# Kernel tuning notes

Measured on AMD Instinct MI355X. Metric: run time of the kernel, lower is better.

## Reference

```python
import jax, jax.numpy as jnp
import numpy as np

D_MODEL = 1024
N_HEADS = 16
D_K = D_MODEL // N_HEADS


def setup_inputs() -> dict:
    key = jax.random.key(0)
    ks = jax.random.split(key, 12)
    B, S = 2, 2048
    scale = 1.0 / np.sqrt(D_MODEL)
    inp = {
        "query": jax.random.normal(ks[0], (B, S, D_MODEL), jnp.float32),
        "key": jax.random.normal(ks[1], (B, S, D_MODEL), jnp.float32),
        "value": jax.random.normal(ks[2], (B, S, D_MODEL), jnp.float32),
        "weights": jax.random.uniform(ks[3], (B, S), jnp.float32),
        "wq": jax.random.normal(ks[4], (D_MODEL, D_MODEL), jnp.float32) * scale,
        "bq": jnp.zeros((D_MODEL,), jnp.float32),
        "wk": jax.random.normal(ks[5], (D_MODEL, D_MODEL), jnp.float32) * scale,
        "bk": jnp.zeros((D_MODEL,), jnp.float32),
        "wv": jax.random.normal(ks[6], (D_MODEL, D_MODEL), jnp.float32) * scale,
        "bv": jnp.zeros((D_MODEL,), jnp.float32),
        "wo": jax.random.normal(ks[7], (D_MODEL, D_MODEL), jnp.float32) * scale,
        "bo": jnp.zeros((D_MODEL,), jnp.float32),
    }
    return inp


def _split_heads(x):
    # (B, S, d_model) -> (B, H, S, d_k)
    B, S, _ = x.shape
    return x.reshape(B, S, N_HEADS, D_K).transpose(0, 2, 1, 3)


def reference(query, key, value, weights, wq, bq, wk, bk, wv, bv, wo, bo):
    Q = _split_heads(query @ wq + bq)
    K = _split_heads(key @ wk + bk)
    V = _split_heads(value @ wv + bv)
    # scores: (B, H, n_q, n_kv)
    scores = jnp.einsum("bhqd,bhkd->bhqk", Q, K) / np.sqrt(D_K)
    log_w = jnp.log(weights + 1e-20)[:, None, None, :]  # (B,1,1,n_kv)
    attn = jax.nn.softmax(scores + log_w, axis=-1)
    out = jnp.einsum("bhqk,bhkd->bhqd", attn, V)
    B, H, S, Dk = out.shape
    out = out.transpose(0, 2, 1, 3).reshape(B, S, D_MODEL)
    return out @ wo + bo
```

## Files before the change

kernel.cpp:

```cpp
#include <hip/hip_runtime.h>

typedef unsigned short u16;
typedef __bf16 bf16x8 __attribute__((ext_vector_type(8)));
typedef float f32x4 __attribute__((ext_vector_type(4)));
typedef float f32x16 __attribute__((ext_vector_type(16)));

#define D_MODEL 1024
#define NH 16
#define DKD 64
#define BB 2
#define SS 2048
#define QSCL 0.18033688011112042f

#if __has_builtin(__builtin_amdgcn_exp2f)
#define EXP2(x) __builtin_amdgcn_exp2f(x)
#else
#define EXP2(x) exp2f(x)
#endif

__device__ __forceinline__ u16 f2bf(float f) {
  union { float f; unsigned u; } x; x.f = f;
  unsigned r = x.u + 0x7fffu + ((x.u >> 16) & 1u);
  return (u16)(r >> 16);
}

__device__ __forceinline__ void gld16(const u16* g, u16* l) {
  __builtin_amdgcn_global_load_lds((__attribute__((address_space(1))) void*)(g),
                                   (__attribute__((address_space(3))) void*)(l),
                                   16, 0, 0);
}

extern "C" __global__ void __launch_bounds__(256) kprep(
    const float* __restrict__ q, const float* __restrict__ k, const float* __restrict__ v,
    const float* __restrict__ wts,
    const float* __restrict__ w0, const float* __restrict__ w1,
    const float* __restrict__ w2, const float* __restrict__ w3,
    u16* __restrict__ xq, u16* __restrict__ xk, u16* __restrict__ xv,
    float* __restrict__ lw,
    u16* __restrict__ o0, u16* __restrict__ o1, u16* __restrict__ o2, u16* __restrict__ o3)
{
  int bx = blockIdx.x;
  if (bx < 12288) {
    int z = bx >> 12, blk = bx & 4095;
    const float* s = z == 0 ? q : (z == 1 ? k : v);
    u16* d = z == 0 ? xq : (z == 1 ? xk : xv);
    int i = (blk * 256 + threadIdx.x) * 4;
    float4 val = *(const float4*)(s + i);
    ushort4 o;
    o.x = f2bf(val.x); o.y = f2bf(val.y); o.z = f2bf(val.z); o.w = f2bf(val.w);
    *(ushort4*)(d + i) = o;
  } else if (bx == 12288) {
    int i = threadIdx.x * 16;
    #pragma unroll
    for (int j = 0; j < 16; j += 4) {
      float4 val = *(const float4*)(wts + i + j);
      lw[i + j + 0] = log2f(val.x + 1e-20f) - 16.0f;
      lw[i + j + 1] = log2f(val.y + 1e-20f) - 16.0f;
      lw[i + j + 2] = log2f(val.z + 1e-20f) - 16.0f;
      lw[i + j + 3] = log2f(val.w + 1e-20f) - 16.0f;
    }
  } else {
    int idx = bx - 12289;
    int wi = idx >> 10, rem = idx & 1023;
    int xb = rem & 31, yb = rem >> 5;
    const float* src; u16* dst;
    switch (wi) {
      case 0: src = w0; dst = o0; break;
      case 1: src = w1; dst = o1; break;
      case 2: src = w2; dst = o2; break;
      default: src = w3; dst = o3; break;
    }
    __shared__ float t[32][33];
    int n0 = xb * 32, k0 = yb * 32;
    int tx = threadIdx.x & 31, ty = threadIdx.x >> 5;
    #pragma unroll
    for (int i = 0; i < 32; i += 8)
      t[ty + i][tx] = src[(k0 + ty + i) * D_MODEL + n0 + tx];
    __syncthreads();
    #pragma unroll
    for (int i = 0; i < 32; i += 8)
      dst[(size_t)(n0 + ty + i) * D_MODEL + k0 + tx] = f2bf(t[tx][ty + i]);
  }
}

__device__ __forceinline__ void gemm_tile(const u16* __restrict__ Ag, const u16* __restrict__ Bg,
                                          u16* As, u16* Bs, f32x4 acc[4][4], int tid)
{
  int lane = tid & 63;
  int lr = lane & 15, lg = lane >> 4;
  int w = tid >> 6, wr = w >> 1, wc = w & 1;
  int sr7 = lr & 7;
  for (int k0 = 0; k0 < D_MODEL; k0 += 64) {
    #pragma unroll
    for (int c = 0; c < 4; ++c) {
      int idx = tid + c * 256;
      int row = idx >> 3, c3 = idx & 7;
      int col = (c3 ^ (row & 7)) * 8;
      gld16(Ag + row * D_MODEL + k0 + col, As + idx * 8);
      gld16(Bg + row * D_MODEL + k0 + col, Bs + idx * 8);
    }
    __syncthreads();
    #pragma unroll
    for (int kk = 0; kk < 2; ++kk) {
      bf16x8 af[4], bfr[4];
      #pragma unroll
      for (int mi = 0; mi < 4; ++mi)
        af[mi] = *(const bf16x8*)(As + (wr * 64 + mi * 16 + lr) * 64 + (((kk * 4 + lg) ^ sr7) * 8));
      #pragma unroll
      for (int nj = 0; nj < 4; ++nj)
        bfr[nj] = *(const bf16x8*)(Bs + (wc * 64 + nj * 16 + lr) * 64 + (((kk * 4 + lg) ^ sr7) * 8));
      #pragma unroll
      for (int mi = 0; mi < 4; ++mi)
        #pragma unroll
        for (int nj = 0; nj < 4; ++nj)
          acc[mi][nj] = __builtin_amdgcn_mfma_f32_16x16x32_bf16(af[mi], bfr[nj], acc[mi][nj], 0, 0, 0);
    }
    __syncthreads();
  }
}

extern "C" __global__ void __launch_bounds__(256) kgemm_qkv(
    const u16* __restrict__ xq, const u16* __restrict__ xk, const u16* __restrict__ xv,
    const u16* __restrict__ wqt, const u16* __restrict__ wkt, const u16* __restrict__ wvt,
    const float* __restrict__ bq, const float* __restrict__ bk, const float* __restrict__ bv,
    u16* __restrict__ Qb, u16* __restrict__ Kb, u16* __restrict__ Vtt)
{
  __shared__ __align__(16) u16 SH[17408];
  u16* As = SH;
  u16* Bs = SH + 8192;
  int z = blockIdx.z;
  const u16* X  = z == 0 ? xq : (z == 1 ? xk : xv);
  const u16* Wt = z == 0 ? wqt : (z == 1 ? wkt : wvt);
  const float* bias = z == 0 ? bq : (z == 1 ? bk : bv);
  int tid = threadIdx.x;
  f32x4 zero = {0.f, 0.f, 0.f, 0.f};
  f32x4 acc[4][4];
  #pragma unroll
  for (int i = 0; i < 4; ++i)
    #pragma unroll
    for (int j = 0; j < 4; ++j) acc[i][j] = zero;
  int m0 = blockIdx.y * 128, n0 = blockIdx.x * 128;
  gemm_tile(X + (size_t)m0 * D_MODEL, Wt + (size_t)n0 * D_MODEL, As, Bs, acc, tid);

  int lane = tid & 63, lr = lane & 15, lg = lane >> 4;
  int w = tid >> 6, wr = w >> 1, wc = w & 1;
  float scl = (z == 0) ? QSCL : 1.0f;

  if (z == 2) {
    #pragma unroll
    for (int mi = 0; mi < 4; ++mi)
      #pragma unroll
      for (int nj = 0; nj < 4; ++nj) {
        int nl = wc * 64 + nj * 16 + lr;
        float bs = bias[n0 + nl];
        int ml = wr * 64 + mi * 16 + lg * 4;
        ushort4 o;
        o.x = f2bf(acc[mi][nj][0] + bs);
        o.y = f2bf(acc[mi][nj][1] + bs);
        o.z = f2bf(acc[mi][nj][2] + bs);
        o.w = f2bf(acc[mi][nj][3] + bs);
        *(ushort4*)&SH[nl * 136 + ml] = o;
      }
    __syncthreads();
    #pragma unroll
    for (int p = 0; p < 8; ++p) {
      int idx = p * 256 + tid;
      int nl = idx >> 4, c = idx & 15;
      int nn = n0 + nl;
      int h = nn >> 6, dk = nn & 63;
      int m = m0 + c * 8;
      int b = m0 >> 11;
      bf16x8 v = *(const bf16x8*)&SH[nl * 136 + c * 8];
      *(bf16x8*)&Vtt[(((size_t)(b * NH + h)) * DKD + dk) * SS + (m & 2047)] = v;
    }
  } else {
    u16* dst = (z == 0) ? Qb : Kb;
    #pragma unroll
    for (int mi = 0; mi < 4; ++mi)
      #pragma unroll
      for (int nj = 0; nj < 4; ++nj) {
        int nl = wc * 64 + nj * 16 + lr;
        float bs = bias[n0 + nl];
        int ml = wr * 64 + mi * 16 + lg * 4;
        #pragma unroll
        for (int j = 0; j < 4; ++j)
          SH[(ml + j) * 136 + nl] = f2bf((acc[mi][nj][j] + bs) * scl);
      }
    __syncthreads();
    #pragma unroll
    for (int p = 0; p < 8; ++p) {
      int idx = p * 256 + tid;
      int ml = idx >> 4, c = idx & 15;
      int m = m0 + ml;
      int b = m >> 11, s = m & 2047;
      int nn = n0 + c * 8;
      int h = nn >> 6, dk = nn & 63;
      bf16x8 v = *(const bf16x8*)&SH[ml * 136 + c * 8];
      *(bf16x8*)&dst[(((size_t)(b * NH + h)) * SS + s) * DKD + dk] = v;
    }
  }
}

extern "C" __global__ void __launch_bounds__(256) kgemm_o(
    const u16* __restrict__ AO, const u16* __restrict__ wot,
    const float* __restrict__ bo, float* __restrict__ out)
{
  __shared__ u16 As[64 * 64], Bs[128 * 64];
  int tid = threadIdx.x;
  int lane = tid & 63, lr = lane & 15, lg = lane >> 4;
  int w = tid >> 6, wr = w & 1, wc = w >> 1;
  int sr7 = lr & 7;
  int m0 = blockIdx.y * 64, n0 = blockIdx.x * 128;
  const u16* Ag = AO + (size_t)m0 * D_MODEL;
  const u16* Bg = wot + (size_t)n0 * D_MODEL;
  f32x4 zero = {0.f, 0.f, 0.f, 0.f};
  f32x4 acc[2][4];
  #pragma unroll
  for (int i = 0; i < 2; ++i)
    #pragma unroll
    for (int j = 0; j < 4; ++j) acc[i][j] = zero;

  for (int k0 = 0; k0 < D_MODEL; k0 += 64) {
    #pragma unroll
    for (int c = 0; c < 2; ++c) {
      int idx = tid + c * 256;
      int row = idx >> 3, c3 = idx & 7;
      int col = (c3 ^ (row & 7)) * 8;
      gld16(Ag + row * D_MODEL + k0 + col, As + idx * 8);
    }
    #pragma unroll
    for (int c = 0; c < 4; ++c) {
      int idx = tid + c * 256;
      int row = idx >> 3, c3 = idx & 7;
      int col = (c3 ^ (row & 7)) * 8;
      gld16(Bg + row * D_MODEL + k0 + col, Bs + idx * 8);
    }
    __syncthreads();
    #pragma unroll
    for (int kk = 0; kk < 2; ++kk) {
      bf16x8 af[2], bfr[4];
      #pragma unroll
      for (int mi = 0; mi < 2; ++mi)
        af[mi] = *(const bf16x8*)(As + (wr * 32 + mi * 16 + lr) * 64 + (((kk * 4 + lg) ^ sr7) * 8));
      #pragma unroll
      for (int nj = 0; nj < 4; ++nj)
        bfr[nj] = *(const bf16x8*)(Bs + (wc * 64 + nj * 16 + lr) * 64 + (((kk * 4 + lg) ^ sr7) * 8));
      #pragma unroll
      for (int mi = 0; mi < 2; ++mi)
        #pragma unroll
        for (int nj = 0; nj < 4; ++nj)
          acc[mi][nj] = __builtin_amdgcn_mfma_f32_16x16x32_bf16(af[mi], bfr[nj], acc[mi][nj], 0, 0, 0);
    }
    __syncthreads();
  }

  #pragma unroll
  for (int mi = 0; mi < 2; ++mi)
    #pragma unroll
    for (int nj = 0; nj < 4; ++nj) {
      int n = n0 + wc * 64 + nj * 16 + lr;
      float bs = bo[n];
      #pragma unroll
      for (int j = 0; j < 4; ++j) {
        int m = m0 + wr * 32 + mi * 16 + lg * 4 + j;
        out[(size_t)m * D_MODEL + n] = acc[mi][nj][j] + bs;
      }
    }
}

extern "C" __global__ void __launch_bounds__(512, 4) kattn(
    const u16* __restrict__ Qb, const u16* __restrict__ Kb, const u16* __restrict__ Vt,
    const float* __restrict__ lw2, u16* __restrict__ AO)
{
  __shared__ __align__(16) char smem[4 * 16384 + 8192];
  float* lwf = (float*)(smem + 65536);

  int tid = threadIdx.x, lane = tid & 63, w = tid >> 6;
  int lq = lane & 31, hi = lane >> 5;
  int qw = w & 3, par = w >> 2;

  int n = blockIdx.x;
  int xcd = n & 7, slot = n >> 3;
  int bh = xcd + 8 * (slot >> 4);
  int q0 = (slot & 15) * 128;
  int b = bh >> 4, h = bh & 15;

  const u16* Qg = Qb + ((size_t)bh * SS + q0 + qw * 32) * DKD;
  const u16* Kg = Kb + (size_t)bh * SS * DKD;
  const u16* Vg = Vt + (size_t)bh * DKD * SS;
  const float* lwb = lw2 + b * SS;

  *(float4*)&lwf[tid * 4] = *(const float4*)(lwb + tid * 4);

  bf16x8 qf[4];
  #pragma unroll
  for (int kc = 0; kc < 4; ++kc)
    qf[kc] = *(const bf16x8*)(Qg + lq * DKD + kc * 16 + hi * 8);

  f32x16 acco[2] = {};
  float lsp[4] = {0.f, 0.f, 0.f, 0.f};

  int srow = tid >> 3, sc = ((tid & 7) ^ (srow & 7)) * 8;

#define KSLOT(sl) ((u16*)(smem + (sl) * 16384))
#define VSLOT(sl) ((u16*)(smem + (sl) * 16384 + 8192))
#define STAGE(t, sl) do { \
    gld16(Kg + (size_t)((t) * 64 + srow) * DKD + sc, KSLOT(sl) + tid * 8); \
    gld16(Vg + (size_t)srow * SS + (t) * 64 + sc, VSLOT(sl) + tid * 8); \
  } while (0)

  STAGE(0, 0); STAGE(1, 1);
  for (int i = 0; i < 16; ++i) {
    asm volatile("s_waitcnt vmcnt(0) lgkmcnt(0)" ::: "memory");
    __builtin_amdgcn_s_barrier();
    __builtin_amdgcn_sched_barrier(0);
    int tn = 2 * i + 2;
    if (tn < 32) { STAGE(tn, tn & 3); STAGE(tn + 1, (tn + 1) & 3); }

    int t = 2 * i + par;
    int sl = t & 3;
    const u16* Kp = KSLOT(sl);
    const u16* Vp = VSLOT(sl);
    int kv0 = t * 64;

    f32x16 st[2];
    #pragma unroll
    for (int nh = 0; nh < 2; ++nh)
      #pragma unroll
      for (int g = 0; g < 4; ++g) {
        f32x4 lv = *(const f32x4*)&lwf[kv0 + nh * 32 + 4 * hi + 8 * g];
        st[nh][4 * g + 0] = lv[0]; st[nh][4 * g + 1] = lv[1];
        st[nh][4 * g + 2] = lv[2]; st[nh][4 * g + 3] = lv[3];
      }

    __builtin_amdgcn_s_setprio(1);
    #pragma unroll
    for (int kc = 0; kc < 4; ++kc) {
      bf16x8 kf0 = *(const bf16x8*)&Kp[(lq) * 64      + (((kc * 2 + hi) ^ (lq & 7)) * 8)];
      bf16x8 kf1 = *(const bf16x8*)&Kp[(32 + lq) * 64 + (((kc * 2 + hi) ^ (lq & 7)) * 8)];
      st[0] = __builtin_amdgcn_mfma_f32_32x32x16_bf16(kf0, qf[kc], st[0], 0, 0, 0);
      st[1] = __builtin_amdgcn_mfma_f32_32x32x16_bf16(kf1, qf[kc], st[1], 0, 0, 0);
    }
    __builtin_amdgcn_s_setprio(0);

    unsigned wd[2][8];
    #pragma unroll
    for (int nh = 0; nh < 2; ++nh)
      #pragma unroll
      for (int r2 = 0; r2 < 8; ++r2) {
        float plo = EXP2(st[nh][2 * r2]);
        float phi = EXP2(st[nh][2 * r2 + 1]);
        lsp[r2 & 3] += plo + phi;
        union { unsigned u; __bf16 b2[2]; } cv;
        cv.b2[0] = (__bf16)plo; cv.b2[1] = (__bf16)phi;
        wd[nh][r2] = cv.u;
      }

    bf16x8 Pb[4];
    #pragma unroll
    for (int c = 0; c < 4; ++c) {
      int nh = c >> 1, j0 = 4 * (c & 1);
      auto s1 = __builtin_amdgcn_permlane32_swap(wd[nh][j0 + 0], wd[nh][j0 + 2], false, false);
      auto s2 = __builtin_amdgcn_permlane32_swap(wd[nh][j0 + 1], wd[nh][j0 + 3], false, false);
      union { unsigned u[4]; bf16x8 v; } pb;
      pb.u[0] = s1[0]; pb.u[1] = s2[0]; pb.u[2] = s1[1]; pb.u[3] = s2[1];
      Pb[c] = pb.v;
    }

    __builtin_amdgcn_s_setprio(1);
    #pragma unroll
    for (int c = 0; c < 4; ++c) {
      bf16x8 vf0 = *(const bf16x8*)&Vp[(lq) * 64      + (((c * 2 + hi) ^ (lq & 7)) * 8)];
      bf16x8 vf1 = *(const bf16x8*)&Vp[(32 + lq) * 64 + (((c * 2 + hi) ^ (lq & 7)) * 8)];
      acco[0] = __builtin_amdgcn_mfma_f32_32x32x16_bf16(vf0, Pb[c], acco[0], 0, 0, 0);
      acco[1] = __builtin_amdgcn_mfma_f32_32x32x16_bf16(vf1, Pb[c], acco[1], 0, 0, 0);
    }
    __builtin_amdgcn_s_setprio(0);
  }
#undef STAGE

  __syncthreads();
  float lsum_part = (lsp[0] + lsp[1]) + (lsp[2] + lsp[3]);
  float* comb = (float*)smem;
  int coff = (qw * 64 + lane) * 34;
  if (par == 1) {
    #pragma unroll
    for (int d = 0; d < 2; ++d)
      #pragma unroll
      for (int g = 0; g < 8; ++g)
        *(float2*)&comb[coff + (d * 8 + g) * 2] = make_float2(acco[d][2 * g], acco[d][2 * g + 1]);
    comb[coff + 32] = lsum_part;
  }
  __syncthreads();
  if (par == 0) {
    #pragma unroll
    for (int d = 0; d < 2; ++d)
      #pragma unroll
      for (int g = 0; g < 8; ++g) {
        float2 v = *(const float2*)&comb[coff + (d * 8 + g) * 2];
        acco[d][2 * g] += v.x; acco[d][2 * g + 1] += v.y;
      }
    lsum_part += comb[coff + 32];
    float lsum = lsum_part + __shfl_xor(lsum_part, 32);
    float inv = 1.0f / lsum;
    int s = q0 + qw * 32 + lq;
    size_t base = ((size_t)b * SS + s) * D_MODEL + h * DKD;
    #pragma unroll
    for (int dh = 0; dh < 2; ++dh)
      #pragma unroll
      for (int g = 0; g < 4; ++g) {
        ushort4 o;
        o.x = f2bf(acco[dh][4 * g + 0] * inv);
        o.y = f2bf(acco[dh][4 * g + 1] * inv);
        o.z = f2bf(acco[dh][4 * g + 2] * inv);
        o.w = f2bf(acco[dh][4 * g + 3] * inv);
        *(ushort4*)(AO + base + dh * 32 + 4 * hi + 8 * g) = o;
      }
  }
#undef KSLOT
#undef VSLOT
}

extern "C" void kernel_launch(void* const* d_in, const int* in_sizes, int n_in,
                              void* d_out, int out_size, void* d_ws, size_t ws_size,
                              hipStream_t stream) {
  const float* query = (const float*)d_in[0];
  const float* key_  = (const float*)d_in[1];
  const float* value = (const float*)d_in[2];
  const float* wts   = (const float*)d_in[3];
  const float* wq = (const float*)d_in[4];
  const float* bq = (const float*)d_in[5];
  const float* wk = (const float*)d_in[6];
  const float* bk = (const float*)d_in[7];
  const float* wv = (const float*)d_in[8];
  const float* bv = (const float*)d_in[9];
  const float* wo = (const float*)d_in[10];
  const float* bo = (const float*)d_in[11];
  float* out = (float*)d_out;

  char* ws = (char*)d_ws;
  const size_t MB = 1024 * 1024;
  u16* Xq  = (u16*)(ws + 0 * MB);
  u16* Xk  = (u16*)(ws + 8 * MB);
  u16* Xv  = (u16*)(ws + 16 * MB);
  u16* WqT = (u16*)(ws + 24 * MB);
  u16* WkT = (u16*)(ws + 26 * MB);
  u16* WvT = (u16*)(ws + 28 * MB);
  u16* WoT = (u16*)(ws + 30 * MB);
  u16* Qb  = (u16*)(ws + 32 * MB);
  u16* Kb  = (u16*)(ws + 40 * MB);
  u16* VtT = (u16*)(ws + 48 * MB);
  u16* AO  = (u16*)(ws + 56 * MB);
  float* lwbuf = (float*)(ws + 64 * MB);

  kprep<<<16385, 256, 0, stream>>>(query, key_, value, wts, wq, wk, wv, wo,
                                   Xq, Xk, Xv, lwbuf, WqT, WkT, WvT, WoT);
  kgemm_qkv<<<dim3(8, 32, 3), 256, 0, stream>>>(Xq, Xk, Xv, WqT, WkT, WvT, bq, bk, bv, Qb, Kb, VtT);
  kattn<<<512, 512, 0, stream>>>(Qb, Kb, VtT, lwbuf, AO);
  kgemm_o<<<dim3(8, 64), 256, 0, stream>>>(AO, WoT, bo, out);
}
```

Baseline: 125.8 us.

## Double-buffer LDS tiles in QKV and output projection GEMMs

Both projection GEMMs now keep two LDS stages. The global-to-LDS loads for the next k-slice are issued right after the barrier and run while the MFMAs consume the current slice, so the per-iteration barrier pairs become a single waitcnt+barrier. The aim is to overlap memory latency with compute. In exchange LDS use roughly doubles (64KB for the QKV kernel, 48KB for the output kernel), which can lower occupancy.

```diff
diff --git a/kernel.cpp b/kernel.cpp
--- a/kernel.cpp
+++ b/kernel.cpp
@@ -83,69 +83,72 @@
   }
 }
 
-__device__ __forceinline__ void gemm_tile(const u16* __restrict__ Ag, const u16* __restrict__ Bg,
-                                          u16* As, u16* Bs, f32x4 acc[4][4], int tid)
-{
-  int lane = tid & 63;
-  int lr = lane & 15, lg = lane >> 4;
-  int w = tid >> 6, wr = w >> 1, wc = w & 1;
-  int sr7 = lr & 7;
-  for (int k0 = 0; k0 < D_MODEL; k0 += 64) {
-    #pragma unroll
-    for (int c = 0; c < 4; ++c) {
-      int idx = tid + c * 256;
-      int row = idx >> 3, c3 = idx & 7;
-      int col = (c3 ^ (row & 7)) * 8;
-      gld16(Ag + row * D_MODEL + k0 + col, As + idx * 8);
-      gld16(Bg + row * D_MODEL + k0 + col, Bs + idx * 8);
-    }
-    __syncthreads();
-    #pragma unroll
-    for (int kk = 0; kk < 2; ++kk) {
-      bf16x8 af[4], bfr[4];
-      #pragma unroll
-      for (int mi = 0; mi < 4; ++mi)
-        af[mi] = *(const bf16x8*)(As + (wr * 64 + mi * 16 + lr) * 64 + (((kk * 4 + lg) ^ sr7) * 8));
-      #pragma unroll
-      for (int nj = 0; nj < 4; ++nj)
-        bfr[nj] = *(const bf16x8*)(Bs + (wc * 64 + nj * 16 + lr) * 64 + (((kk * 4 + lg) ^ sr7) * 8));
-      #pragma unroll
-      for (int mi = 0; mi < 4; ++mi)
-        #pragma unroll
-        for (int nj = 0; nj < 4; ++nj)
-          acc[mi][nj] = __builtin_amdgcn_mfma_f32_16x16x32_bf16(af[mi], bfr[nj], acc[mi][nj], 0, 0, 0);
-    }
-    __syncthreads();
-  }
-}
-
 extern "C" __global__ void __launch_bounds__(256) kgemm_qkv(
     const u16* __restrict__ xq, const u16* __restrict__ xk, const u16* __restrict__ xv,
     const u16* __restrict__ wqt, const u16* __restrict__ wkt, const u16* __restrict__ wvt,
     const float* __restrict__ bq, const float* __restrict__ bk, const float* __restrict__ bv,
     u16* __restrict__ Qb, u16* __restrict__ Kb, u16* __restrict__ Vtt)
 {
-  __shared__ __align__(16) u16 SH[17408];
-  u16* As = SH;
-  u16* Bs = SH + 8192;
+  __shared__ __align__(16) u16 SH[32768];
   int z = blockIdx.z;
   const u16* X  = z == 0 ? xq : (z == 1 ? xk : xv);
   const u16* Wt = z == 0 ? wqt : (z == 1 ? wkt : wvt);
   const float* bias = z == 0 ? bq : (z == 1 ? bk : bv);
   int tid = threadIdx.x;
+  int m0 = blockIdx.y * 128, n0 = blockIdx.x * 128;
+  const u16* Ag = X + (size_t)m0 * D_MODEL;
+  const u16* Bg = Wt + (size_t)n0 * D_MODEL;
+
+  int lane = tid & 63, lr = lane & 15, lg = lane >> 4;
+  int w = tid >> 6, wr = w >> 1, wc = w & 1;
+  int sr7 = lr & 7;
+
   f32x4 zero = {0.f, 0.f, 0.f, 0.f};
   f32x4 acc[4][4];
   #pragma unroll
   for (int i = 0; i < 4; ++i)
     #pragma unroll
     for (int j = 0; j < 4; ++j) acc[i][j] = zero;
-  int m0 = blockIdx.y * 128, n0 = blockIdx.x * 128;
-  gemm_tile(X + (size_t)m0 * D_MODEL, Wt + (size_t)n0 * D_MODEL, As, Bs, acc, tid);
-
-  int lane = tid & 63, lr = lane & 15, lg = lane >> 4;
-  int w = tid >> 6, wr = w >> 1, wc = w & 1;
+
+#define GSTAGE(k0, base) do { \
+    _Pragma("unroll") \
+    for (int c = 0; c < 4; ++c) { \
+      int idx = tid + c * 256; \
+      int row = idx >> 3, c3 = idx & 7; \
+      int col = (c3 ^ (row & 7)) * 8; \
+      gld16(Ag + row * D_MODEL + (k0) + col, SH + (base) + idx * 8); \
+      gld16(Bg + row * D_MODEL + (k0) + col, SH + (base) + 8192 + idx * 8); \
+    } \
+  } while (0)
+
+  GSTAGE(0, 0);
+  for (int ks = 0; ks < 16; ++ks) {
+    asm volatile("s_waitcnt vmcnt(0) lgkmcnt(0)" ::: "memory");
+    __builtin_amdgcn_s_barrier();
+    __builtin_amdgcn_sched_barrier(0);
+    if (ks + 1 < 16) GSTAGE((ks + 1) * 64, ((ks + 1) & 1) * 16384);
+    const u16* Asp = SH + (ks & 1) * 16384;
+    const u16* Bsp = Asp + 8192;
+    #pragma unroll
+    for (int kk = 0; kk < 2; ++kk) {
+      bf16x8 af[4], bfr[4];
+      #pragma unroll
+      for (int mi = 0; mi < 4; ++mi)
+        af[mi] = *(const bf16x8*)(Asp + (wr * 64 + mi * 16 + lr) * 64 + (((kk * 4 + lg) ^ sr7) * 8));
+      #pragma unroll
+      for (int nj = 0; nj < 4; ++nj)
+        bfr[nj] = *(const bf16x8*)(Bsp + (wc * 64 + nj * 16 + lr) * 64 + (((kk * 4 + lg) ^ sr7) * 8));
+      #pragma unroll
+      for (int mi = 0; mi < 4; ++mi)
+        #pragma unroll
+        for (int nj = 0; nj < 4; ++nj)
+          acc[mi][nj] = __builtin_amdgcn_mfma_f32_16x16x32_bf16(af[mi], bfr[nj], acc[mi][nj], 0, 0, 0);
+    }
+  }
+#undef GSTAGE
+  __syncthreads();
+
   float scl = (z == 0) ? QSCL : 1.0f;
-
   if (z == 2) {
     #pragma unroll
     for (int mi = 0; mi < 4; ++mi)
@@ -170,8 +173,8 @@
       int h = nn >> 6, dk = nn & 63;
       int m = m0 + c * 8;
       int b = m0 >> 11;
-      bf16x8 v = *(const bf16x8*)&SH[nl * 136 + c * 8];
-      *(bf16x8*)&Vtt[(((size_t)(b * NH + h)) * DKD + dk) * SS + (m & 2047)] = v;
+      bf16x8 vv = *(const bf16x8*)&SH[nl * 136 + c * 8];
+      *(bf16x8*)&Vtt[(((size_t)(b * NH + h)) * DKD + dk) * SS + (m & 2047)] = vv;
     }
   } else {
     u16* dst = (z == 0) ? Qb : Kb;
@@ -195,8 +198,8 @@
       int b = m >> 11, s = m & 2047;
       int nn = n0 + c * 8;
       int h = nn >> 6, dk = nn & 63;
-      bf16x8 v = *(const bf16x8*)&SH[ml * 136 + c * 8];
-      *(bf16x8*)&dst[(((size_t)(b * NH + h)) * SS + s) * DKD + dk] = v;
+      bf16x8 vv = *(const bf16x8*)&SH[ml * 136 + c * 8];
+      *(bf16x8*)&dst[(((size_t)(b * NH + h)) * SS + s) * DKD + dk] = vv;
     }
   }
 }
@@ -205,7 +208,7 @@
     const u16* __restrict__ AO, const u16* __restrict__ wot,
     const float* __restrict__ bo, float* __restrict__ out)
 {
-  __shared__ u16 As[64 * 64], Bs[128 * 64];
+  __shared__ __align__(16) u16 SH[24576];
   int tid = threadIdx.x;
   int lane = tid & 63, lr = lane & 15, lg = lane >> 4;
   int w = tid >> 6, wr = w & 1, wc = w >> 1;
@@ -220,39 +223,48 @@
     #pragma unroll
     for (int j = 0; j < 4; ++j) acc[i][j] = zero;
 
-  for (int k0 = 0; k0 < D_MODEL; k0 += 64) {
-    #pragma unroll
-    for (int c = 0; c < 2; ++c) {
-      int idx = tid + c * 256;
-      int row = idx >> 3, c3 = idx & 7;
-      int col = (c3 ^ (row & 7)) * 8;
-      gld16(Ag + row * D_MODEL + k0 + col, As + idx * 8);
-    }
-    #pragma unroll
-    for (int c = 0; c < 4; ++c) {
-      int idx = tid + c * 256;
-      int row = idx >> 3, c3 = idx & 7;
-      int col = (c3 ^ (row & 7)) * 8;
-      gld16(Bg + row * D_MODEL + k0 + col, Bs + idx * 8);
-    }
-    __syncthreads();
+#define OSTAGE(k0, base) do { \
+    _Pragma("unroll") \
+    for (int c = 0; c < 2; ++c) { \
+      int idx = tid + c * 256; \
+      int row = idx >> 3, c3 = idx & 7; \
+      int col = (c3 ^ (row & 7)) * 8; \
+      gld16(Ag + row * D_MODEL + (k0) + col, SH + (base) + idx * 8); \
+    } \
+    _Pragma("unroll") \
+    for (int c = 0; c < 4; ++c) { \
+      int idx = tid + c * 256; \
+      int row = idx >> 3, c3 = idx & 7; \
+      int col = (c3 ^ (row & 7)) * 8; \
+      gld16(Bg + row * D_MODEL + (k0) + col, SH + (base) + 4096 + idx * 8); \
+    } \
+  } while (0)
+
+  OSTAGE(0, 0);
+  for (int ks = 0; ks < 16; ++ks) {
+    asm volatile("s_waitcnt vmcnt(0) lgkmcnt(0)" ::: "memory");
+    __builtin_amdgcn_s_barrier();
+    __builtin_amdgcn_sched_barrier(0);
+    if (ks + 1 < 16) OSTAGE((ks + 1) * 64, ((ks + 1) & 1) * 12288);
+    const u16* Asp = SH + (ks & 1) * 12288;
+    const u16* Bsp = Asp + 4096;
     #pragma unroll
     for (int kk = 0; kk < 2; ++kk) {
       bf16x8 af[2], bfr[4];
       #pragma unroll
       for (int mi = 0; mi < 2; ++mi)
-        af[mi] = *(const bf16x8*)(As + (wr * 32 + mi * 16 + lr) * 64 + (((kk * 4 + lg) ^ sr7) * 8));
+        af[mi] = *(const bf16x8*)(Asp + (wr * 32 + mi * 16 + lr) * 64 + (((kk * 4 + lg) ^ sr7) * 8));
       #pragma unroll
       for (int nj = 0; nj < 4; ++nj)
-        bfr[nj] = *(const bf16x8*)(Bs + (wc * 64 + nj * 16 + lr) * 64 + (((kk * 4 + lg) ^ sr7) * 8));
+        bfr[nj] = *(const bf16x8*)(Bsp + (wc * 64 + nj * 16 + lr) * 64 + (((kk * 4 + lg) ^ sr7) * 8));
       #pragma unroll
       for (int mi = 0; mi < 2; ++mi)
         #pragma unroll
         for (int nj = 0; nj < 4; ++nj)
           acc[mi][nj] = __builtin_amdgcn_mfma_f32_16x16x32_bf16(af[mi], bfr[nj], acc[mi][nj], 0, 0, 0);
     }
-    __syncthreads();
-  }
+  }
+#undef OSTAGE
 
   #pragma unroll
   for (int mi = 0; mi < 2; ++mi)
```

New measurement: 121.0 us. 1.04x faster.
